# Performance work log

Hardware: AMD Instinct MI355X
Metric: run time of the kernel (lower is better)

Reference implementation:

```python
import jax, jax.numpy as jnp
import numpy as np

B, S, IN = 4, 4096, 2048
E, D, A, R = 16, 128, 128, 4  # num_experts, expert_vector_dim, attn_dim, mlp_rank
LN_EPS = 1e-5


def _ln2(x, g, b):
    # LayerNorm over the last two dims [E, D] jointly (torch nn.LayerNorm([E, D]))
    mu = x.mean(axis=(-2, -1), keepdims=True)
    var = ((x - mu) ** 2).mean(axis=(-2, -1), keepdims=True)
    return (x - mu) * jax.lax.rsqrt(var + LN_EPS) * g + b


def setup_inputs() -> dict:
    key = jax.random.key(0)
    ks = jax.random.split(key, 8)
    f32 = jnp.float32
    return {
        "hidden_states": jax.random.normal(ks[0], (B, S, IN), f32),
        "expert_embedding": jax.random.normal(ks[1], (E, D), f32) * 0.02,
        "ln_gamma": jnp.ones((E, D), f32),
        "ln_beta": jnp.zeros((E, D), f32),
        "Wv_w": jax.random.normal(ks[2], (E, IN), f32) * 0.02,
        "Wv_b": jnp.zeros((E,), f32),
        "mlp_w1": jax.random.normal(ks[3], (R, IN), f32) * 0.02,
        "mlp_b1": jnp.zeros((R,), f32),
        "mlp_w2": jax.random.normal(ks[4], (E * D, R), f32) * 0.02,
        "mlp_b2": jnp.zeros((E * D,), f32),
        "te_Wq": jax.random.normal(ks[5], (A, D), f32) * 0.05,
        "te_Wk": jax.random.normal(ks[6], (A, D), f32) * 0.05,
        "top_k": 2,
    }


def reference(hidden_states, expert_embedding, ln_gamma, ln_beta, Wv_w, Wv_b,
              mlp_w1, mlp_b1, mlp_w2, mlp_b2, te_Wq, te_Wk, top_k):
    # global expert vectors, layernormed over [E, D]: (E, D)
    ge = _ln2(expert_embedding[None, None], ln_gamma, ln_beta)[0, 0]
    # input gate = W_v(hidden): (B, S, E)
    input_gate = jnp.einsum('bsi,ei->bse', hidden_states, Wv_w) + Wv_b
    # TE mlp -> dynamic per-token expert vectors: (B, S, E, D)
    h = jax.nn.relu(jnp.einsum('bsi,ri->bsr', hidden_states, mlp_w1) + mlp_b1)
    dyn = (jnp.einsum('bsr,or->bso', h, mlp_w2) + mlp_b2).reshape(B, S, E, D)
    dyn = _ln2(dyn, ln_gamma, ln_beta)
    # attention-style routing: Q from dyn experts, K from global experts
    q = jnp.einsum('bsed,ad->bsea', dyn, te_Wq)     # (B, S, E, A)
    k = jnp.einsum('ed,ad->ea', ge, te_Wk)          # (E, A)
    scale = 1.0 / float(np.sqrt(A))
    sim = jax.nn.softmax(jnp.einsum('bsqa,ka->bsqk', q, k) * scale, axis=-1)
    gate = jnp.einsum('bsqk,bsk->bsq', sim, input_gate)
    rw = jax.nn.softmax(gate, axis=-1)              # (B, S, E)
    # top-k masking + sharpened softmax (temperature 0.1)
    vals, idx = jax.lax.top_k(rw, top_k)            # (B, S, k)
    oh = jax.nn.one_hot(idx, E, dtype=rw.dtype)     # (B, S, k, E)
    scattered = jnp.einsum('bske,bsk->bse', oh, vals)
    keep = oh.sum(axis=-2) > 0
    neg = jnp.finfo(rw.dtype).min
    masked = jnp.where(keep, scattered, neg)
    return jax.nn.softmax(masked / 0.1, axis=-1)
```

## Files before the change

### kernel.cpp

```cpp
#include <hip/hip_runtime.h>
#include <math.h>

#define NTOK   16384
#define INDIM  2048
#define NROWS  20
#define CHUNK  256

#define WS_PKT  0
#define WS_D1K  1024
#define WS_GQK  1280
#define WS_BQK  1536
#define WS_SCAL 1792
#define WS_TOT  1818

#define SIM_SCALE 0.08838834764831845f

#define LBUF1   5120
#define LRED2_STRIDE 324
#define LRED    5440

__device__ __forceinline__ void async16(const float* g, float* l) {
    __builtin_amdgcn_global_load_lds(
        (const __attribute__((address_space(1))) void*)g,
        (__attribute__((address_space(3))) void*)l, 16, 0, 0);
}

__device__ __forceinline__ void stage_rows(const float* __restrict__ wv,
                                           const float* __restrict__ w1,
                                           float* ldsbase, int wave, int lane,
                                           int goff) {
    const int l4 = lane << 2;
    #pragma unroll
    for (int j = 0; j < 5; ++j) {
        const int r = wave + (j << 2);
        const float* src = (j < 4) ? (wv + (r << 11)) : (w1 + ((r - 16) << 11));
        async16(src + goff + l4, ldsbase + r * CHUNK + l4);
    }
}

__device__ __forceinline__ void load_h(float4* hr, const float* hb, int c) {
    const float* p = hb + (c << 8);
    hr[0] = *(const float4*)(p);
    hr[1] = *(const float4*)(p + INDIM);
    hr[2] = *(const float4*)(p + 2 * INDIM);
    hr[3] = *(const float4*)(p + 3 * INDIM);
}

__device__ __forceinline__ void compute_chunk(float acc[NROWS][4],
                                              const float* wb,
                                              const float4 h[4]) {
    #pragma unroll
    for (int w = 0; w < NROWS; ++w) {
        float4 wf = *(const float4*)(wb + (w << 8));
        #pragma unroll
        for (int t = 0; t < 4; ++t) {
            acc[w][t] = fmaf(h[t].x, wf.x,
                        fmaf(h[t].y, wf.y,
                        fmaf(h[t].z, wf.z,
                        fmaf(h[t].w, wf.w, acc[w][t]))));
        }
    }
}

__global__ __launch_bounds__(256) void hr_pre2(
    const float* __restrict__ ee, const float* __restrict__ gam,
    const float* __restrict__ bta, const float* __restrict__ w2,
    const float* __restrict__ b2, const float* __restrict__ wq,
    const float* __restrict__ wk, float* __restrict__ ws)
{
    const int tid  = threadIdx.x;
    const int bx   = blockIdx.x;
    const int lane = tid & 63;
    const int wave = tid >> 6;

    if (bx == 16) {
        __shared__ float sacc[26];
        if (tid < 26) sacc[tid] = 0.f;
        __syncthreads();
        float pa[26];
        #pragma unroll
        for (int j = 0; j < 26; ++j) pa[j] = 0.f;
        for (int i = tid; i < 2048; i += 256) {
            float b = b2[i];
            float4 w4 = *(const float4*)(w2 + i * 4);
            float wr[4] = {w4.x, w4.y, w4.z, w4.w};
            pa[0] += b;
            pa[1] += b * b;
            #pragma unroll
            for (int r = 0; r < 4; ++r) {
                pa[2 + r] += wr[r];
                pa[6 + r] += b * wr[r];
                #pragma unroll
                for (int r2 = 0; r2 < 4; ++r2) pa[10 + r * 4 + r2] += wr[r] * wr[r2];
            }
        }
        #pragma unroll
        for (int j = 0; j < 26; ++j) {
            float v = pa[j];
            v += __shfl_xor(v, 32); v += __shfl_xor(v, 16); v += __shfl_xor(v, 8);
            v += __shfl_xor(v, 4);  v += __shfl_xor(v, 2);  v += __shfl_xor(v, 1);
            if (lane == 0) atomicAdd(&sacc[j], v);
        }
        __syncthreads();
        if (tid < 26) ws[WS_SCAL + tid] = sacc[tid] * (1.f / 2048.f);
        return;
    }

    const int e2 = bx;
    __shared__ float sge[128];
    __shared__ float sK[128];
    __shared__ float sWqK[128];
    __shared__ float sred[8];

    float v8[8];
    float s = 0.f;
    #pragma unroll
    for (int j = 0; j < 8; ++j) { v8[j] = ee[tid + j * 256]; s += v8[j]; }
    s += __shfl_xor(s, 32); s += __shfl_xor(s, 16); s += __shfl_xor(s, 8);
    s += __shfl_xor(s, 4);  s += __shfl_xor(s, 2);  s += __shfl_xor(s, 1);
    if (lane == 0) sred[wave] = s;
    __syncthreads();
    const float mu = (sred[0] + sred[1] + sred[2] + sred[3]) * (1.f / 2048.f);
    float q = 0.f;
    #pragma unroll
    for (int j = 0; j < 8; ++j) { float d = v8[j] - mu; q += d * d; }
    q += __shfl_xor(q, 32); q += __shfl_xor(q, 16); q += __shfl_xor(q, 8);
    q += __shfl_xor(q, 4);  q += __shfl_xor(q, 2);  q += __shfl_xor(q, 1);
    if (lane == 0) sred[4 + wave] = q;
    __syncthreads();
    const float rsq = rsqrtf((sred[4] + sred[5] + sred[6] + sred[7]) * (1.f / 2048.f) + 1e-5f);

    if (tid < 128) {
        int idx = (e2 << 7) + tid;
        sge[tid] = (ee[idx] - mu) * rsq * gam[idx] + bta[idx];
    }
    __syncthreads();

    {
        int a = tid >> 1, half = tid & 1;
        const float* wr = wk + (a << 7) + (half << 6);
        const float* gg = sge + (half << 6);
        float acc = 0.f;
        #pragma unroll 8
        for (int j = 0; j < 64; ++j) acc = fmaf(gg[j], wr[j], acc);
        acc += __shfl_xor(acc, 1);
        if (half == 0) sK[a] = acc;
    }
    __syncthreads();

    {
        int d = tid >> 1, half = tid & 1;
        float acc = 0.f;
        #pragma unroll 8
        for (int j = 0; j < 64; ++j) {
            int a = (half << 6) + j;
            acc = fmaf(wq[(a << 7) + d], sK[a], acc);
        }
        acc += __shfl_xor(acc, 1);
        if (half == 0) sWqK[d] = acc;
    }
    __syncthreads();

    {
        int o = tid >> 2, qd = tid & 3;
        int r = o >> 4, e = o & 15;
        float acc = 0.f;
        #pragma unroll 8
        for (int j = 0; j < 32; ++j) {
            int d  = (qd << 5) + j;
            int ed = (e << 7) + d;
            acc = fmaf(w2[ed * 4 + r] * gam[ed], sWqK[d], acc);
        }
        acc += __shfl_xor(acc, 1);
        acc += __shfl_xor(acc, 2);
        if (qd == 0) ws[WS_PKT + (e2 << 6) + (r << 4) + e] = acc;
    }

    if (tid < 192) {
        int kind = tid >> 6;
        int e    = (tid >> 2) & 15;
        int qd   = tid & 3;
        float acc = 0.f;
        #pragma unroll 8
        for (int j = 0; j < 32; ++j) {
            int d  = (qd << 5) + j;
            int ed = (e << 7) + d;
            float w = sWqK[d];
            float t = (kind == 0) ? b2[ed] * gam[ed]
                    : (kind == 1) ? gam[ed]
                                  : bta[ed];
            acc = fmaf(t, w, acc);
        }
        acc += __shfl_xor(acc, 1);
        acc += __shfl_xor(acc, 2);
        if (qd == 0) ws[WS_D1K + (kind << 8) + (e2 << 4) + e] = acc;
    }
}

__global__ __launch_bounds__(256) void hr_main(
    const float* __restrict__ hidden, const float* __restrict__ wv,
    const float* __restrict__ wvb, const float* __restrict__ w1,
    const float* __restrict__ b1, const float* __restrict__ tab,
    float* __restrict__ out)
{
    __shared__ float lds[10240];

    const int tid  = threadIdx.x;
    const int wave = tid >> 6;
    const int lane = tid & 63;
    const int tok0 = (blockIdx.x << 4) + (wave << 2);
    const float* hb = hidden + (size_t)tok0 * INDIM + (lane << 2);

    float acc[NROWS][4];
    #pragma unroll
    for (int w = 0; w < NROWS; ++w) {
        acc[w][0] = 0.f; acc[w][1] = 0.f; acc[w][2] = 0.f; acc[w][3] = 0.f;
    }

    float4 ha[4];
    stage_rows(wv, w1, lds, wave, lane, 0);
    load_h(ha, hb, 0);
    __syncthreads();

    for (int cc = 0; cc < 4; ++cc) {
        const int c1 = 2 * cc + 1;
        stage_rows(wv, w1, lds + LBUF1, wave, lane, c1 << 8);
        compute_chunk(acc, &lds[lane << 2], ha);
        load_h(ha, hb, c1);
        __syncthreads();
        if (cc != 3) stage_rows(wv, w1, lds, wave, lane, (c1 + 1) << 8);
        compute_chunk(acc, &lds[LBUF1 + (lane << 2)], ha);
        if (cc != 3) load_h(ha, hb, c1 + 1);
        __syncthreads();
    }

    #pragma unroll
    for (int w = 0; w < NROWS; ++w) {
        #pragma unroll
        for (int t = 0; t < 4; ++t) {
            float v = acc[w][t];
            v += __shfl_xor(v, 32);
            v += __shfl_xor(v, 16);
            acc[w][t] = v;
        }
    }
    {
        const int q = lane >> 4, i = lane & 15;
        #pragma unroll
        for (int w = 0; w < NROWS; ++w) {
            if (q == w / 5) {
                #pragma unroll
                for (int t = 0; t < 4; ++t)
                    lds[((wave << 2) + t) * LRED2_STRIDE + (w << 4) + i] = acc[w][t];
            }
        }
    }
    __syncthreads();

    #pragma unroll
    for (int pp = 0; pp < 2; ++pp) {
        const int p = tid + pp * 256;
        if (p < 320) {
            const int w = p >> 4, tok = p & 15;
            const float4* rp = (const float4*)&lds[tok * LRED2_STRIDE + (w << 4)];
            float4 r0 = rp[0], r1 = rp[1], r2 = rp[2], r3 = rp[3];
            float s = (r0.x + r0.y + r0.z + r0.w) + (r1.x + r1.y + r1.z + r1.w)
                    + (r2.x + r2.y + r2.z + r2.w) + (r3.x + r3.y + r3.z + r3.w);
            lds[LRED + tok * 20 + w] = s;
        }
    }
    __syncthreads();

    const int tok = tid >> 4;
    const int e   = tid & 15;

    float ig[16];
    #pragma unroll
    for (int j = 0; j < 16; ++j) ig[j] = lds[LRED + tok * 20 + j] + wvb[j];
    float h[4];
    #pragma unroll
    for (int r = 0; r < 4; ++r) h[r] = fmaxf(lds[LRED + tok * 20 + 16 + r] + b1[r], 0.f);

    float muT = tab[WS_SCAL + 0];
    float e2m = tab[WS_SCAL + 1];
    #pragma unroll
    for (int r = 0; r < 4; ++r) {
        muT = fmaf(h[r], tab[WS_SCAL + 2 + r], muT);
        e2m = fmaf(2.f * h[r], tab[WS_SCAL + 6 + r], e2m);
        #pragma unroll
        for (int r2 = 0; r2 < 4; ++r2)
            e2m = fmaf(h[r] * h[r2], tab[WS_SCAL + 10 + r * 4 + r2], e2m);
    }
    const float var = e2m - muT * muT;
    const float rsq = rsqrtf(var + 1e-5f);

    float sv[16];
    #pragma unroll
    for (int e2 = 0; e2 < 16; ++e2) {
        float s = tab[WS_D1K + (e2 << 4) + e];
        s = fmaf(h[0], tab[(e2 << 6) + e], s);
        s = fmaf(h[1], tab[(e2 << 6) + 16 + e], s);
        s = fmaf(h[2], tab[(e2 << 6) + 32 + e], s);
        s = fmaf(h[3], tab[(e2 << 6) + 48 + e], s);
        s = fmaf(-muT, tab[WS_GQK + (e2 << 4) + e], s);
        sv[e2] = (rsq * s + tab[WS_BQK + (e2 << 4) + e]) * SIM_SCALE;
    }
    float mx = sv[0];
    #pragma unroll
    for (int e2 = 1; e2 < 16; ++e2) mx = fmaxf(mx, sv[e2]);
    float den = 0.f, gate = 0.f;
    #pragma unroll
    for (int e2 = 0; e2 < 16; ++e2) {
        float p = __expf(sv[e2] - mx);
        den += p;
        gate = fmaf(p, ig[e2], gate);
    }
    gate /= den;

    float gm = gate;
    gm = fmaxf(gm, __shfl_xor(gm, 1));
    gm = fmaxf(gm, __shfl_xor(gm, 2));
    gm = fmaxf(gm, __shfl_xor(gm, 4));
    gm = fmaxf(gm, __shfl_xor(gm, 8));
    float ex = __expf(gate - gm);
    float es = ex;
    es += __shfl_xor(es, 1);
    es += __shfl_xor(es, 2);
    es += __shfl_xor(es, 4);
    es += __shfl_xor(es, 8);
    const float rw = ex / es;

    float v1 = rw; int i1 = e;
    #pragma unroll
    for (int m = 1; m <= 8; m <<= 1) {
        float ov = __shfl_xor(v1, m);
        int   oi = __shfl_xor(i1, m);
        if (ov > v1 || (ov == v1 && oi < i1)) { v1 = ov; i1 = oi; }
    }
    float v2 = (e == i1) ? -INFINITY : rw; int i2 = e;
    #pragma unroll
    for (int m = 1; m <= 8; m <<= 1) {
        float ov = __shfl_xor(v2, m);
        int   oi = __shfl_xor(i2, m);
        if (ov > v2 || (ov == v2 && oi < i2)) { v2 = ov; i2 = oi; }
    }

    float oval = 0.f;
    if (e == i1 || e == i2) {
        float t = __expf((v2 - v1) * 10.f);
        oval = (e == i1) ? (1.f / (1.f + t)) : (t / (1.f + t));
    }
    out[(((size_t)blockIdx.x << 4) + tok) * 16 + e] = oval;
}

extern "C" void kernel_launch(void* const* d_in, const int* in_sizes, int n_in,
                              void* d_out, int out_size, void* d_ws, size_t ws_size,
                              hipStream_t stream)
{
    const float* hidden = (const float*)d_in[0];
    const float* ee     = (const float*)d_in[1];
    const float* gam    = (const float*)d_in[2];
    const float* bta    = (const float*)d_in[3];
    const float* wv     = (const float*)d_in[4];
    const float* wvb    = (const float*)d_in[5];
    const float* w1     = (const float*)d_in[6];
    const float* b1     = (const float*)d_in[7];
    const float* w2     = (const float*)d_in[8];
    const float* b2     = (const float*)d_in[9];
    const float* wq     = (const float*)d_in[10];
    const float* wk     = (const float*)d_in[11];
    float* out = (float*)d_out;
    float* ws  = (float*)d_ws;

    hipLaunchKernelGGL(hr_pre2, dim3(17), dim3(256), 0, stream,
                       ee, gam, bta, w2, b2, wq, wk, ws);
    hipLaunchKernelGGL(hr_main, dim3(NTOK / 16), dim3(256), 0, stream,
                       hidden, wv, wvb, w1, b1, ws, out);
}
```

Baseline: 263.4 us.

## Let each wave stage all weight rows and replace syncthreads with raw barriers

Each wave now issues async global-to-LDS copies for all 20 weight rows of a chunk, rather than a quarter of them. All four waves write identical data into named double buffers wtA and wtB. The hidden-state prefetch is split into current and next register sets. Full __syncthreads are replaced with an lgkmcnt wait, s_barrier and sched_barrier, aiming to cut barrier cost and let loads overlap compute. The cost is four times as many LDS-DMA instructions and global reads. The wait also does not cover vmcnt, so correctness depends on the compiler inserting waits for the async LDS loads. The reduction scratch reuses the weight buffers.

```diff
diff --git a/kernel.cpp b/kernel.cpp
--- a/kernel.cpp
+++ b/kernel.cpp
@@ -15,9 +15,7 @@
 
 #define SIM_SCALE 0.08838834764831845f
 
-#define LBUF1   5120
-#define LRED2_STRIDE 324
-#define LRED    5440
+#define WAITCNT_LGKM0 0xC07F
 
 __device__ __forceinline__ void async16(const float* g, float* l) {
     __builtin_amdgcn_global_load_lds(
@@ -25,17 +23,15 @@
         (__attribute__((address_space(3))) void*)l, 16, 0, 0);
 }
 
-__device__ __forceinline__ void stage_rows(const float* __restrict__ wv,
-                                           const float* __restrict__ w1,
-                                           float* ldsbase, int wave, int lane,
-                                           int goff) {
-    const int l4 = lane << 2;
-    #pragma unroll
-    for (int j = 0; j < 5; ++j) {
-        const int r = wave + (j << 2);
-        const float* src = (j < 4) ? (wv + (r << 11)) : (w1 + ((r - 16) << 11));
-        async16(src + goff + l4, ldsbase + r * CHUNK + l4);
-    }
+__device__ __forceinline__ void stage_w(const float* __restrict__ wv,
+                                        const float* __restrict__ w1,
+                                        float* dst, int goff, int l4) {
+    #pragma unroll
+    for (int r = 0; r < 16; ++r)
+        async16(wv + (r << 11) + goff + l4, dst + r * CHUNK + l4);
+    #pragma unroll
+    for (int r = 0; r < 4; ++r)
+        async16(w1 + (r << 11) + goff + l4, dst + ((16 + r) * CHUNK) + l4);
 }
 
 __device__ __forceinline__ void load_h(float4* hr, const float* hb, int c) {
@@ -203,13 +199,16 @@
     const float* __restrict__ b1, const float* __restrict__ tab,
     float* __restrict__ out)
 {
-    __shared__ float lds[10240];
+    __shared__ float wtA[NROWS * CHUNK];
+    __shared__ float wtB[NROWS * CHUNK];
+    __shared__ float red2[16 * NROWS];
 
     const int tid  = threadIdx.x;
     const int wave = tid >> 6;
     const int lane = tid & 63;
+    const int l4   = lane << 2;
     const int tok0 = (blockIdx.x << 4) + (wave << 2);
-    const float* hb = hidden + (size_t)tok0 * INDIM + (lane << 2);
+    const float* hb = hidden + (size_t)tok0 * INDIM + l4;
 
     float acc[NROWS][4];
     #pragma unroll
@@ -217,22 +216,29 @@
         acc[w][0] = 0.f; acc[w][1] = 0.f; acc[w][2] = 0.f; acc[w][3] = 0.f;
     }
 
-    float4 ha[4];
-    stage_rows(wv, w1, lds, wave, lane, 0);
-    load_h(ha, hb, 0);
-    __syncthreads();
+    float4 hcur[4], hnxt[4];
+    stage_w(wv, w1, wtA, 0, l4);
+    load_h(hcur, hb, 0);
 
     for (int cc = 0; cc < 4; ++cc) {
         const int c1 = 2 * cc + 1;
-        stage_rows(wv, w1, lds + LBUF1, wave, lane, c1 << 8);
-        compute_chunk(acc, &lds[lane << 2], ha);
-        load_h(ha, hb, c1);
-        __syncthreads();
-        if (cc != 3) stage_rows(wv, w1, lds, wave, lane, (c1 + 1) << 8);
-        compute_chunk(acc, &lds[LBUF1 + (lane << 2)], ha);
-        if (cc != 3) load_h(ha, hb, c1 + 1);
-        __syncthreads();
-    }
+        stage_w(wv, w1, wtB, c1 << 8, l4);
+        load_h(hnxt, hb, c1);
+        compute_chunk(acc, &wtA[l4], hcur);
+        __builtin_amdgcn_s_waitcnt(WAITCNT_LGKM0);
+        __builtin_amdgcn_s_barrier();
+        __builtin_amdgcn_sched_barrier(0);
+        if (cc != 3) {
+            stage_w(wv, w1, wtA, (c1 + 1) << 8, l4);
+            load_h(hcur, hb, c1 + 1);
+        }
+        compute_chunk(acc, &wtB[l4], hnxt);
+        __builtin_amdgcn_s_waitcnt(WAITCNT_LGKM0);
+        __builtin_amdgcn_s_barrier();
+        __builtin_amdgcn_sched_barrier(0);
+    }
+
+    __syncthreads();
 
     #pragma unroll
     for (int w = 0; w < NROWS; ++w) {
@@ -249,9 +255,11 @@
         #pragma unroll
         for (int w = 0; w < NROWS; ++w) {
             if (q == w / 5) {
+                float* buf = (w < 10) ? wtA : wtB;
+                const int wi = (w < 10) ? w : (w - 10);
                 #pragma unroll
                 for (int t = 0; t < 4; ++t)
-                    lds[((wave << 2) + t) * LRED2_STRIDE + (w << 4) + i] = acc[w][t];
+                    buf[((wave << 2) + t) * 160 + wi * 16 + i] = acc[w][t];
             }
         }
     }
@@ -259,14 +267,16 @@
 
     #pragma unroll
     for (int pp = 0; pp < 2; ++pp) {
-        const int p = tid + pp * 256;
+        const int p = tid + (pp << 8);
         if (p < 320) {
             const int w = p >> 4, tok = p & 15;
-            const float4* rp = (const float4*)&lds[tok * LRED2_STRIDE + (w << 4)];
+            const float* buf = (w < 10) ? wtA : wtB;
+            const int wi = (w < 10) ? w : (w - 10);
+            const float4* rp = (const float4*)&buf[tok * 160 + wi * 16];
             float4 r0 = rp[0], r1 = rp[1], r2 = rp[2], r3 = rp[3];
             float s = (r0.x + r0.y + r0.z + r0.w) + (r1.x + r1.y + r1.z + r1.w)
                     + (r2.x + r2.y + r2.z + r2.w) + (r3.x + r3.y + r3.z + r3.w);
-            lds[LRED + tok * 20 + w] = s;
+            red2[tok * NROWS + w] = s;
         }
     }
     __syncthreads();
@@ -276,10 +286,10 @@
 
     float ig[16];
     #pragma unroll
-    for (int j = 0; j < 16; ++j) ig[j] = lds[LRED + tok * 20 + j] + wvb[j];
+    for (int j = 0; j < 16; ++j) ig[j] = red2[tok * NROWS + j] + wvb[j];
     float h[4];
     #pragma unroll
-    for (int r = 0; r < 4; ++r) h[r] = fmaxf(lds[LRED + tok * 20 + 16 + r] + b1[r], 0.f);
+    for (int r = 0; r < 4; ++r) h[r] = fmaxf(red2[tok * NROWS + 16 + r] + b1[r], 0.f);
 
     float muT = tab[WS_SCAL + 0];
     float e2m = tab[WS_SCAL + 1];
```

Result: faster. 248.8 us (-5.5%).
